# Performance work log

Measured on AMD Instinct MI355X. Metric: run time of the kernel, lower is better.

## Reference

```python
import jax, jax.numpy as jnp
import numpy as np

N, D, M = 2048, 512, 8

def setup_inputs() -> dict:
    key = jax.random.key(0)
    kx, ka = jax.random.split(key)
    X = jax.random.normal(kx, (N, D), dtype=jnp.float32)
    A = jax.random.normal(ka, (M, N, N), dtype=jnp.float32)
    return {"X": X, "A": A, "K": 8}

def reference(X, A, K):
    # Y = X X^T : [N, N]
    Y = X @ X.T
    for _ in range(K):
        # trace(A_m^T Y) == sum(A_m * Y)  (elementwise dot, avoids O(N^3) matmul)
        scores = jnp.einsum('mij,ij->m', A, Y)                 # [M]
        component = jnp.einsum('m,mij->ij', scores, A)         # [N, N]
        denominator = jnp.sum(component * component)           # trace(C^T C)
        numerator = jnp.sum(component * Y)                     # trace(C^T Y)
        Y = Y - (numerator / denominator) * component
        # beta_m = trace(A_m^T C) / den ; original updates A every iteration
        beta = jnp.einsum('mij,ij->m', A, component) / denominator  # [M]
        A = A - beta[:, None, None] * component
    return Y
```

## Files before the change

### kernel.cpp

```cpp
#include <hip/hip_runtime.h>

#define NN 2048
#define DD 512
#define MM 8
#define GRAM_BLOCKS 2048

typedef __attribute__((ext_vector_type(8))) short short8_t;
typedef __attribute__((ext_vector_type(4))) float f32x4_t;

#define AS1 __attribute__((address_space(1)))
#define AS3 __attribute__((address_space(3)))

__host__ __device__ constexpr int tri_idx(int m, int mm) {
    return m * 8 - m * (m + 1) / 2 + mm;
}

__device__ inline unsigned short f2bf_rne(float f) {
    unsigned int u = __float_as_uint(f);
    u += 0x7FFFu + ((u >> 16) & 1u);
    return (unsigned short)(u >> 16);
}
__device__ inline float bf2f(unsigned short h) {
    return __uint_as_float(((unsigned int)h) << 16);
}

__global__ __launch_bounds__(256) void convert_split(const float* __restrict__ X,
                                                     unsigned short* __restrict__ Xhi,
                                                     unsigned short* __restrict__ Xlo) {
    const int idx = (blockIdx.x * 256 + threadIdx.x) * 4;
    float4 v = *reinterpret_cast<const float4*>(&X[idx]);
    float xs[4] = {v.x, v.y, v.z, v.w};
    ushort4 hi, lo;
    unsigned short* hp = &hi.x;
    unsigned short* lp = &lo.x;
    #pragma unroll
    for (int j = 0; j < 4; ++j) {
        unsigned short h = f2bf_rne(xs[j]);
        hp[j] = h;
        lp[j] = f2bf_rne(xs[j] - bf2f(h));
    }
    *reinterpret_cast<ushort4*>(&Xhi[idx]) = hi;
    *reinterpret_cast<ushort4*>(&Xlo[idx]) = lo;
}

__global__ __launch_bounds__(256) void gemm_mfma(const unsigned short* __restrict__ Xhi,
                                                 const unsigned short* __restrict__ Xlo,
                                                 float* __restrict__ Y) {
    __shared__ unsigned short lds[4 * 128 * 32];
    unsigned short* bufs[4] = {lds, lds + 4096, lds + 8192, lds + 12288};

    const int tid = threadIdx.x;
    const int lane = tid & 63;
    const int wave = tid >> 6;
    const int wr = wave >> 1;
    const int wc = wave & 1;
    const int rowBase = blockIdx.y * 128;
    const int colBase = blockIdx.x * 128;

    f32x4_t acc[4][4] = {};

    const int r = lane & 15;
    const int gq = lane >> 4;

    for (int k0 = 0; k0 < DD; k0 += 32) {
        __syncthreads();
        #pragma unroll
        for (int i = 0; i < 2; ++i) {
            const int gc = i * 256 + tid;
            const int row = gc >> 2;
            const int g = gc & 3;
            const int gsrc = g ^ ((row >> 1) & 3);
            const unsigned short* gA = &Xhi[(rowBase + row) * DD + k0 + gsrc * 8];
            const unsigned short* gAl = &Xlo[(rowBase + row) * DD + k0 + gsrc * 8];
            const unsigned short* gB = &Xhi[(colBase + row) * DD + k0 + gsrc * 8];
            const unsigned short* gBl = &Xlo[(colBase + row) * DD + k0 + gsrc * 8];
            const int lbase = (i * 256 + wave * 64) * 8;
            __builtin_amdgcn_global_load_lds((const AS1 unsigned int*)gA,
                                             (AS3 unsigned int*)(bufs[0] + lbase), 16, 0, 0);
            __builtin_amdgcn_global_load_lds((const AS1 unsigned int*)gAl,
                                             (AS3 unsigned int*)(bufs[1] + lbase), 16, 0, 0);
            __builtin_amdgcn_global_load_lds((const AS1 unsigned int*)gB,
                                             (AS3 unsigned int*)(bufs[2] + lbase), 16, 0, 0);
            __builtin_amdgcn_global_load_lds((const AS1 unsigned int*)gBl,
                                             (AS3 unsigned int*)(bufs[3] + lbase), 16, 0, 0);
        }
        __syncthreads();

        short8_t ah[4], al[4], bh[4], bl[4];
        #pragma unroll
        for (int m = 0; m < 4; ++m) {
            const int row = wr * 64 + m * 16 + r;
            const int off = row * 32 + ((gq ^ ((row >> 1) & 3)) * 8);
            ah[m] = *reinterpret_cast<const short8_t*>(&bufs[0][off]);
            al[m] = *reinterpret_cast<const short8_t*>(&bufs[1][off]);
        }
        #pragma unroll
        for (int n = 0; n < 4; ++n) {
            const int row = wc * 64 + n * 16 + r;
            const int off = row * 32 + ((gq ^ ((row >> 1) & 3)) * 8);
            bh[n] = *reinterpret_cast<const short8_t*>(&bufs[2][off]);
            bl[n] = *reinterpret_cast<const short8_t*>(&bufs[3][off]);
        }
        #pragma unroll
        for (int m = 0; m < 4; ++m) {
            #pragma unroll
            for (int n = 0; n < 4; ++n) {
                acc[m][n] = __builtin_amdgcn_mfma_f32_16x16x32_bf16(ah[m], bh[n], acc[m][n], 0, 0, 0);
                acc[m][n] = __builtin_amdgcn_mfma_f32_16x16x32_bf16(ah[m], bl[n], acc[m][n], 0, 0, 0);
                acc[m][n] = __builtin_amdgcn_mfma_f32_16x16x32_bf16(al[m], bh[n], acc[m][n], 0, 0, 0);
            }
        }
    }

    #pragma unroll
    for (int m = 0; m < 4; ++m) {
        #pragma unroll
        for (int n = 0; n < 4; ++n) {
            #pragma unroll
            for (int j = 0; j < 4; ++j) {
                const int rr = rowBase + wr * 64 + m * 16 + gq * 4 + j;
                const int cc = colBase + wc * 64 + n * 16 + r;
                Y[rr * NN + cc] = acc[m][n][j];
            }
        }
    }
}

__global__ __launch_bounds__(256) void gram_kernel(const float* __restrict__ A,
                                                   const float* __restrict__ Y,
                                                   float* __restrict__ partialT) {
    const int P4 = (NN * NN) / 4;
    float vals[44];
    #pragma unroll
    for (int i = 0; i < 44; ++i) vals[i] = 0.f;

    const float4* Y4 = reinterpret_cast<const float4*>(Y);
    const float4* A4 = reinterpret_cast<const float4*>(A);
    const int base = blockIdx.x * 512 + threadIdx.x;

    #pragma unroll
    for (int it = 0; it < 2; ++it) {
        const int p = base + it * 256;
        float4 y = Y4[p];
        float4 a[MM];
        #pragma unroll
        for (int m = 0; m < MM; ++m) a[m] = A4[m * P4 + p];
        #pragma unroll
        for (int m = 0; m < MM; ++m) {
            vals[36 + m] += a[m].x * y.x + a[m].y * y.y + a[m].z * y.z + a[m].w * y.w;
            #pragma unroll
            for (int mm = m; mm < MM; ++mm) {
                vals[tri_idx(m, mm)] += a[m].x * a[mm].x + a[m].y * a[mm].y +
                                        a[m].z * a[mm].z + a[m].w * a[mm].w;
            }
        }
    }

    #pragma unroll
    for (int i = 0; i < 44; ++i) {
        float v = vals[i];
        #pragma unroll
        for (int off = 32; off > 0; off >>= 1) v += __shfl_down(v, off);
        vals[i] = v;
    }

    __shared__ float wsum[4][44];
    const int lane = threadIdx.x & 63;
    const int wv = threadIdx.x >> 6;
    if (lane == 0) {
        #pragma unroll
        for (int i = 0; i < 44; ++i) wsum[wv][i] = vals[i];
    }
    __syncthreads();
    if (threadIdx.x < 44) {
        float s = wsum[0][threadIdx.x] + wsum[1][threadIdx.x] +
                  wsum[2][threadIdx.x] + wsum[3][threadIdx.x];
        partialT[threadIdx.x * GRAM_BLOCKS + blockIdx.x] = s;
    }
}

__global__ __launch_bounds__(256) void gram_reduce(const float* __restrict__ partialT,
                                                   float* __restrict__ acc) {
    const int v = blockIdx.x;
    float s = 0.f;
    for (int b = threadIdx.x; b < GRAM_BLOCKS; b += 256)
        s += partialT[v * GRAM_BLOCKS + b];
    #pragma unroll
    for (int off = 32; off > 0; off >>= 1) s += __shfl_down(s, off);

    __shared__ float wsum[4];
    const int lane = threadIdx.x & 63;
    const int wv = threadIdx.x >> 6;
    if (lane == 0) wsum[wv] = s;
    __syncthreads();
    if (threadIdx.x == 0)
        acc[v] = wsum[0] + wsum[1] + wsum[2] + wsum[3];
}

__global__ __launch_bounds__(64, 1) void iterate_kernel(const float* __restrict__ acc,
                                                        const int* __restrict__ Kp,
                                                        float* __restrict__ w_out) {
    double G[MM][MM], s0[MM], T[MM][MM], w[MM];
    #pragma unroll
    for (int m = 0; m < MM; ++m) {
        #pragma unroll
        for (int mm = m; mm < MM; ++mm) {
            double v = (double)acc[tri_idx(m, mm)];
            G[m][mm] = v;
            G[mm][m] = v;
        }
    }
    #pragma unroll
    for (int m = 0; m < MM; ++m) s0[m] = (double)acc[36 + m];
    #pragma unroll
    for (int m = 0; m < MM; ++m) {
        w[m] = 0.0;
        #pragma unroll
        for (int k = 0; k < MM; ++k) T[m][k] = (m == k) ? 1.0 : 0.0;
    }

    const int K = *Kp;
    for (int it = 0; it < K; ++it) {
        double sy[MM];
        #pragma unroll
        for (int k = 0; k < MM; ++k) {
            double a = s0[k];
            #pragma unroll
            for (int j = 0; j < MM; ++j) a += G[k][j] * w[j];
            sy[k] = a;
        }
        double s[MM];
        #pragma unroll
        for (int m = 0; m < MM; ++m) {
            double a = 0.0;
            #pragma unroll
            for (int k = 0; k < MM; ++k) a += T[m][k] * sy[k];
            s[m] = a;
        }
        double c[MM];
        #pragma unroll
        for (int k = 0; k < MM; ++k) {
            double a = 0.0;
            #pragma unroll
            for (int m = 0; m < MM; ++m) a += T[m][k] * s[m];
            c[k] = a;
        }
        double Gc[MM];
        #pragma unroll
        for (int k = 0; k < MM; ++k) {
            double a = 0.0;
            #pragma unroll
            for (int j = 0; j < MM; ++j) a += G[k][j] * c[j];
            Gc[k] = a;
        }
        double den = 0.0, num = 0.0;
        #pragma unroll
        for (int k = 0; k < MM; ++k) den += c[k] * Gc[k];
        #pragma unroll
        for (int m = 0; m < MM; ++m) num += s[m] * s[m];
        const double inv_den = 1.0 / den;
        const double alpha = num * inv_den;
        #pragma unroll
        for (int k = 0; k < MM; ++k) w[k] -= alpha * c[k];
        #pragma unroll
        for (int m = 0; m < MM; ++m) {
            double beta = 0.0;
            #pragma unroll
            for (int k = 0; k < MM; ++k) beta += T[m][k] * Gc[k];
            beta *= inv_den;
            #pragma unroll
            for (int k = 0; k < MM; ++k) T[m][k] -= beta * c[k];
        }
    }
    if (threadIdx.x == 0 && blockIdx.x == 0) {
        #pragma unroll
        for (int k = 0; k < MM; ++k) w_out[k] = (float)w[k];
    }
}

__global__ __launch_bounds__(256) void reconstruct(const float* __restrict__ A,
                                                   const float* __restrict__ w,
                                                   float* __restrict__ Y) {
    __shared__ float wsh[MM];
    if (threadIdx.x < MM) wsh[threadIdx.x] = w[threadIdx.x];
    __syncthreads();
    float wl[MM];
    #pragma unroll
    for (int m = 0; m < MM; ++m) wl[m] = wsh[m];

    const int P4 = (NN * NN) / 4;
    float4* Y4 = reinterpret_cast<float4*>(Y);
    const float4* A4 = reinterpret_cast<const float4*>(A);
    const int base = blockIdx.x * 512 + threadIdx.x;

    #pragma unroll
    for (int it = 0; it < 2; ++it) {
        const int p = base + it * 256;
        float4 y = Y4[p];
        #pragma unroll
        for (int m = 0; m < MM; ++m) {
            float4 a = A4[m * P4 + p];
            y.x += wl[m] * a.x;
            y.y += wl[m] * a.y;
            y.z += wl[m] * a.z;
            y.w += wl[m] * a.w;
        }
        Y4[p] = y;
    }
}

extern "C" void kernel_launch(void* const* d_in, const int* in_sizes, int n_in,
                              void* d_out, int out_size, void* d_ws, size_t ws_size,
                              hipStream_t stream) {
    const float* X = (const float*)d_in[0];
    const float* A = (const float*)d_in[1];
    const int* Kp = (const int*)d_in[2];
    float* Y = (float*)d_out;

    float* acc = (float*)d_ws;
    float* w = acc + 48;
    unsigned short* Xhi = (unsigned short*)((char*)d_ws + 4096);
    unsigned short* Xlo = Xhi + NN * DD;
    float* partialT = (float*)((char*)d_ws + (8u << 20));

    convert_split<<<1024, 256, 0, stream>>>(X, Xhi, Xlo);
    gemm_mfma<<<dim3(16, 16), 256, 0, stream>>>(Xhi, Xlo, Y);
    gram_kernel<<<GRAM_BLOCKS, 256, 0, stream>>>(A, Y, partialT);
    gram_reduce<<<44, 256, 0, stream>>>(partialT, acc);
    iterate_kernel<<<1, 64, 0, stream>>>(acc, Kp, w);
    reconstruct<<<2048, 256, 0, stream>>>(A, w, Y);
}
```

Measured before the change: 106.6 us.

## Double-buffer GEMM LDS staging and fuse gram reduction via last-block atomic

The GEMM now uses two LDS buffers, so the global-to-LDS loads for the next K tile are issued while MFMAs run on the current tile, and one barrier per iteration replaces two. The separate gram_reduce launch is removed: each gram block bumps an atomic counter, and the last block to finish sums the partials into acc. The counter is reset in convert_split. This saves a kernel launch and hides load latency in the GEMM, at the cost of doubling LDS use and running the final reduction serially in a single block.

```diff
diff --git a/kernel.cpp b/kernel.cpp
--- a/kernel.cpp
+++ b/kernel.cpp
@@ -26,7 +26,9 @@
 
 __global__ __launch_bounds__(256) void convert_split(const float* __restrict__ X,
                                                      unsigned short* __restrict__ Xhi,
-                                                     unsigned short* __restrict__ Xlo) {
+                                                     unsigned short* __restrict__ Xlo,
+                                                     int* __restrict__ counter) {
+    if (blockIdx.x == 0 && threadIdx.x == 0) *counter = 0;
     const int idx = (blockIdx.x * 256 + threadIdx.x) * 4;
     float4 v = *reinterpret_cast<const float4*>(&X[idx]);
     float xs[4] = {v.x, v.y, v.z, v.w};
@@ -46,8 +48,7 @@
 __global__ __launch_bounds__(256) void gemm_mfma(const unsigned short* __restrict__ Xhi,
                                                  const unsigned short* __restrict__ Xlo,
                                                  float* __restrict__ Y) {
-    __shared__ unsigned short lds[4 * 128 * 32];
-    unsigned short* bufs[4] = {lds, lds + 4096, lds + 8192, lds + 12288};
+    __shared__ unsigned short lds[2][4 * 128 * 32];
 
     const int tid = threadIdx.x;
     const int lane = tid & 63;
@@ -62,44 +63,52 @@
     const int r = lane & 15;
     const int gq = lane >> 4;
 
-    for (int k0 = 0; k0 < DD; k0 += 32) {
-        __syncthreads();
+    auto stage = [&](int d, int k0) {
+        unsigned short* base = &lds[d][0];
         #pragma unroll
         for (int i = 0; i < 2; ++i) {
             const int gc = i * 256 + tid;
             const int row = gc >> 2;
             const int g = gc & 3;
             const int gsrc = g ^ ((row >> 1) & 3);
-            const unsigned short* gA = &Xhi[(rowBase + row) * DD + k0 + gsrc * 8];
+            const unsigned short* gA  = &Xhi[(rowBase + row) * DD + k0 + gsrc * 8];
             const unsigned short* gAl = &Xlo[(rowBase + row) * DD + k0 + gsrc * 8];
-            const unsigned short* gB = &Xhi[(colBase + row) * DD + k0 + gsrc * 8];
+            const unsigned short* gB  = &Xhi[(colBase + row) * DD + k0 + gsrc * 8];
             const unsigned short* gBl = &Xlo[(colBase + row) * DD + k0 + gsrc * 8];
             const int lbase = (i * 256 + wave * 64) * 8;
             __builtin_amdgcn_global_load_lds((const AS1 unsigned int*)gA,
-                                             (AS3 unsigned int*)(bufs[0] + lbase), 16, 0, 0);
+                                             (AS3 unsigned int*)(base + 0 + lbase), 16, 0, 0);
             __builtin_amdgcn_global_load_lds((const AS1 unsigned int*)gAl,
-                                             (AS3 unsigned int*)(bufs[1] + lbase), 16, 0, 0);
+                                             (AS3 unsigned int*)(base + 4096 + lbase), 16, 0, 0);
             __builtin_amdgcn_global_load_lds((const AS1 unsigned int*)gB,
-                                             (AS3 unsigned int*)(bufs[2] + lbase), 16, 0, 0);
+                                             (AS3 unsigned int*)(base + 8192 + lbase), 16, 0, 0);
             __builtin_amdgcn_global_load_lds((const AS1 unsigned int*)gBl,
-                                             (AS3 unsigned int*)(bufs[3] + lbase), 16, 0, 0);
-        }
-        __syncthreads();
-
+                                             (AS3 unsigned int*)(base + 12288 + lbase), 16, 0, 0);
+        }
+    };
+
+    stage(0, 0);
+    __syncthreads();
+
+    for (int t = 0; t < 16; ++t) {
+        const int cur = t & 1;
+        if (t < 15) stage(cur ^ 1, (t + 1) * 32);
+
+        const unsigned short* base = &lds[cur][0];
         short8_t ah[4], al[4], bh[4], bl[4];
         #pragma unroll
         for (int m = 0; m < 4; ++m) {
             const int row = wr * 64 + m * 16 + r;
             const int off = row * 32 + ((gq ^ ((row >> 1) & 3)) * 8);
-            ah[m] = *reinterpret_cast<const short8_t*>(&bufs[0][off]);
-            al[m] = *reinterpret_cast<const short8_t*>(&bufs[1][off]);
+            ah[m] = *reinterpret_cast<const short8_t*>(&base[0 + off]);
+            al[m] = *reinterpret_cast<const short8_t*>(&base[4096 + off]);
         }
         #pragma unroll
         for (int n = 0; n < 4; ++n) {
             const int row = wc * 64 + n * 16 + r;
             const int off = row * 32 + ((gq ^ ((row >> 1) & 3)) * 8);
-            bh[n] = *reinterpret_cast<const short8_t*>(&bufs[2][off]);
-            bl[n] = *reinterpret_cast<const short8_t*>(&bufs[3][off]);
+            bh[n] = *reinterpret_cast<const short8_t*>(&base[8192 + off]);
+            bl[n] = *reinterpret_cast<const short8_t*>(&base[12288 + off]);
         }
         #pragma unroll
         for (int m = 0; m < 4; ++m) {
@@ -110,6 +119,7 @@
                 acc[m][n] = __builtin_amdgcn_mfma_f32_16x16x32_bf16(al[m], bh[n], acc[m][n], 0, 0, 0);
             }
         }
+        __syncthreads();
     }
 
     #pragma unroll
@@ -128,7 +138,9 @@
 
 __global__ __launch_bounds__(256) void gram_kernel(const float* __restrict__ A,
                                                    const float* __restrict__ Y,
-                                                   float* __restrict__ partialT) {
+                                                   float* __restrict__ partialT,
+                                                   float* __restrict__ acc,
+                                                   int* __restrict__ counter) {
     const int P4 = (NN * NN) / 4;
     float vals[44];
     #pragma unroll
@@ -177,24 +189,25 @@
                   wsum[2][threadIdx.x] + wsum[3][threadIdx.x];
         partialT[threadIdx.x * GRAM_BLOCKS + blockIdx.x] = s;
     }
-}
-
-__global__ __launch_bounds__(256) void gram_reduce(const float* __restrict__ partialT,
-                                                   float* __restrict__ acc) {
-    const int v = blockIdx.x;
-    float s = 0.f;
-    for (int b = threadIdx.x; b < GRAM_BLOCKS; b += 256)
-        s += partialT[v * GRAM_BLOCKS + b];
-    #pragma unroll
-    for (int off = 32; off > 0; off >>= 1) s += __shfl_down(s, off);
-
-    __shared__ float wsum[4];
-    const int lane = threadIdx.x & 63;
-    const int wv = threadIdx.x >> 6;
-    if (lane == 0) wsum[wv] = s;
+
+    __shared__ int amLast;
+    __threadfence();
+    if (threadIdx.x == 0)
+        amLast = (atomicAdd(counter, 1) == GRAM_BLOCKS - 1) ? 1 : 0;
     __syncthreads();
-    if (threadIdx.x == 0)
-        acc[v] = wsum[0] + wsum[1] + wsum[2] + wsum[3];
+    if (amLast) {
+        __threadfence();
+        #pragma unroll
+        for (int q = 0; q < 11; ++q) {
+            const int v = wv * 11 + q;
+            float s = 0.f;
+            for (int b = lane; b < GRAM_BLOCKS; b += 64)
+                s += partialT[v * GRAM_BLOCKS + b];
+            #pragma unroll
+            for (int off = 32; off > 0; off >>= 1) s += __shfl_down(s, off);
+            if (lane == 0) acc[v] = s;
+        }
+    }
 }
 
 __global__ __launch_bounds__(64, 1) void iterate_kernel(const float* __restrict__ acc,
@@ -318,15 +331,15 @@
     float* Y = (float*)d_out;
 
     float* acc = (float*)d_ws;
-    float* w = acc + 48;
+    int* counter = (int*)d_ws + 46;
+    float* w = (float*)d_ws + 48;
     unsigned short* Xhi = (unsigned short*)((char*)d_ws + 4096);
     unsigned short* Xlo = Xhi + NN * DD;
     float* partialT = (float*)((char*)d_ws + (8u << 20));
 
-    convert_split<<<1024, 256, 0, stream>>>(X, Xhi, Xlo);
+    convert_split<<<1024, 256, 0, stream>>>(X, Xhi, Xlo, counter);
     gemm_mfma<<<dim3(16, 16), 256, 0, stream>>>(Xhi, Xlo, Y);
-    gram_kernel<<<GRAM_BLOCKS, 256, 0, stream>>>(A, Y, partialT);
-    gram_reduce<<<44, 256, 0, stream>>>(partialT, acc);
+    gram_kernel<<<GRAM_BLOCKS, 256, 0, stream>>>(A, Y, partialT, acc, counter);
     iterate_kernel<<<1, 64, 0, stream>>>(acc, Kp, w);
     reconstruct<<<2048, 256, 0, stream>>>(A, w, Y);
 }
```

Result: slower. 370.3 us (+247.4%).
